# Kernel optimization log

Hardware: AMD Instinct MI355X
Metric: run time of the kernel (lower is better)

## Reference

```python
import jax, jax.numpy as jnp
import numpy as np

B, S, DM, H, SD = 8, 2048, 512, 8, 64
INNER = H * SD
HID = 4 * DM
EPS = 1e-5


def setup_inputs() -> dict:
    key = jax.random.key(0)
    ks = jax.random.split(key, 12)
    p = lambda k, sh: jax.random.normal(k, sh, dtype=jnp.float32) * 0.02
    return {
        "x": jax.random.normal(ks[0], (B, S, DM), dtype=jnp.float32),
        "norm_g": jnp.ones((DM,), jnp.float32),
        "norm_b": jnp.zeros((DM,), jnp.float32),
        "ffn_norm_g": jnp.ones((DM,), jnp.float32),
        "ffn_norm_b": jnp.zeros((DM,), jnp.float32),
        "Wa": p(ks[1], (INNER, DM)),
        "Wb": p(ks[2], (INNER, DM)),
        "Wql": p(ks[3], (INNER, DM)),
        "Wqr": p(ks[4], (INNER, DM)),
        "Wsd": p(ks[5], (H, DM)),
        "bsd": jnp.zeros((H,), jnp.float32),
        "Wpd": p(ks[6], (H, DM)),
        "bpd": jnp.zeros((H,), jnp.float32),
        "Wout": p(ks[7], (DM, INNER)),
        "W1": p(ks[8], (HID, DM)),
        "b1": jnp.zeros((HID,), jnp.float32),
        "W2": p(ks[9], (DM, HID)),
        "b2": jnp.zeros((DM,), jnp.float32),
    }


def _ln(x, g, b):
    m = x.mean(-1, keepdims=True)
    v = ((x - m) ** 2).mean(-1, keepdims=True)
    return (x - m) / jnp.sqrt(v + EPS) * g + b


def reference(x, norm_g, norm_b, ffn_norm_g, ffn_norm_b, Wa, Wb, Wql, Wqr,
              Wsd, bsd, Wpd, bpd, Wout, W1, b1, W2, b2):
    n = _ln(x, norm_g, norm_b)  # [B,S,DM]
    # project, reshape to heads, move time axis first for scan: [S,B,H,SD]
    tm = lambda t: t.reshape(B, S, H, SD).transpose(1, 0, 2, 3)
    a_all = tm(jnp.tanh(n @ Wa.T))
    b_all = tm(jnp.tanh(n @ Wb.T))
    ql_all = tm(jnp.tanh(n @ Wql.T))
    qr_all = tm(jnp.tanh(n @ Wqr.T))
    sd_all = jax.nn.sigmoid(n @ Wsd.T + bsd).transpose(1, 0, 2)[..., None]        # [S,B,H,1]
    pd_all = jax.nn.sigmoid(n @ Wpd.T + bpd).transpose(1, 0, 2)[..., None, None]  # [S,B,H,1,1]

    def step(carry, inp):
        state, pair = carry  # state [B,H,SD], pair [B,H,SD,SD]
        at, bt, qlt, sdt, pdt = inp
        prev = state
        state = sdt * state + (1.0 - sdt) * at
        pair = pdt * pair + (1.0 - pdt) * jnp.einsum('bhd,bhe->bhde', prev, bt)
        lc = jnp.einsum('bhde,bhd->bhe', pair, qlt)  # left context [B,H,SD]
        return (state, pair), lc

    init = (jnp.zeros((B, H, SD), x.dtype), jnp.zeros((B, H, SD, SD), x.dtype))
    _, lc = jax.lax.scan(step, init, (a_all, b_all, ql_all, sd_all, pd_all))  # [S,B,H,SD]

    mixed = ((lc * qr_all).transpose(1, 0, 2, 3).reshape(B, S, INNER)) @ Wout.T  # [B,S,DM]
    r = x + mixed  # dropout is identity in eval
    h = jax.nn.gelu(_ln(r, ffn_norm_g, ffn_norm_b) @ W1.T + b1, approximate=False)
    return r + h @ W2.T + b2
```

## Files before the change

### kernel.cpp

```cpp
#include <hip/hip_runtime.h>
#include <cstdint>
#include <cstddef>

#define B_    8
#define S_    2048
#define DM_   512
#define H_    8
#define SD_   64
#define HID_  2048
#define ROWS  (B_*S_)
#define BH    (B_*H_)
#define NCHUNK 32
#define CLEN   64
#define EPS_  1e-5f
#define PLANE ((size_t)ROWS*64)

typedef __bf16 bf16x8 __attribute__((ext_vector_type(8)));
typedef float  floatx4 __attribute__((ext_vector_type(4)));


static __device__ __forceinline__ float bf2f(unsigned short h){
  union { unsigned int u; float f; } v; v.u = ((unsigned int)h) << 16; return v.f;
}
static __device__ __forceinline__ unsigned short f2bf(float f){
  union { float f; unsigned int u; } v; v.f = f;
  unsigned int r = v.u + 0x7fffu + ((v.u >> 16) & 1u);
  return (unsigned short)(r >> 16);
}
static __device__ __forceinline__ float fast_tanh(float x){
  float ax = fabsf(x);
  float e  = __expf(2.f*ax);
  float t  = 1.f - 2.f/(e+1.f);
  return copysignf(t, x);
}
static __device__ __forceinline__ float sigmoidf_(float z){
  return 1.f/(1.f + expf(-z));
}
static __device__ __forceinline__ float gelu_exact(float x){
  return 0.5f*x*(1.f + erff(x*0.70710678118654752440f));
}
static __device__ __forceinline__ void gld_lds16(const unsigned short* g, unsigned short* lds){
  __builtin_amdgcn_global_load_lds(
      (const __attribute__((address_space(1))) void*)g,
      (__attribute__((address_space(3))) void*)lds,
      16, 0, 0);
}
static __device__ __forceinline__ int swz(int row, int col){
  return row*64 + (((col>>3) ^ (row&7))<<3) + (col&7);
}

__global__ __launch_bounds__(256) void cvt_weights(
    const float* __restrict__ wa, const float* __restrict__ wb,
    const float* __restrict__ wql, const float* __restrict__ wqr,
    const float* __restrict__ wout, const float* __restrict__ w1,
    const float* __restrict__ w2,
    unsigned short* __restrict__ wcat, unsigned short* __restrict__ woutb,
    unsigned short* __restrict__ w1b, unsigned short* __restrict__ w2b){
  int i = blockIdx.x*256 + threadIdx.x;
  const float* s; unsigned short* d; int base;
  if      (i <  65536){ s=wa;   d=wcat;          base=i; }
  else if (i < 131072){ s=wb;   d=wcat+262144;   base=i-65536; }
  else if (i < 196608){ s=wql;  d=wcat+524288;   base=i-131072; }
  else if (i < 262144){ s=wqr;  d=wcat+786432;   base=i-196608; }
  else if (i < 327680){ s=wout; d=woutb;         base=i-262144; }
  else if (i < 589824){ s=w1;   d=w1b;           base=i-327680; }
  else                { s=w2;   d=w2b;           base=i-589824; }
  float4 v = ((const float4*)s)[base];
  ushort4 o; o.x=f2bf(v.x); o.y=f2bf(v.y); o.z=f2bf(v.z); o.w=f2bf(v.w);
  ((ushort4*)d)[base] = o;
}

__global__ __launch_bounds__(256) void ln_gates(
    const float* __restrict__ x, const float* __restrict__ gam, const float* __restrict__ bet,
    const float* __restrict__ Wsd, const float* __restrict__ bsd,
    const float* __restrict__ Wpd, const float* __restrict__ bpd,
    unsigned short* __restrict__ nbf, float* __restrict__ sdo, float* __restrict__ pdo){
  const int row = blockIdx.x*4 + (threadIdx.x>>6), l = threadIdx.x & 63;
  const float* xr = x + (size_t)row*DM_;
  float4 v0 = ((const float4*)xr)[l*2];
  float4 v1 = ((const float4*)xr)[l*2+1];
  float v[8] = {v0.x,v0.y,v0.z,v0.w,v1.x,v1.y,v1.z,v1.w};
  float s = 0.f;
  #pragma unroll
  for (int i=0;i<8;++i) s += v[i];
  #pragma unroll
  for (int m=1;m<64;m<<=1) s += __shfl_xor(s, m);
  const float mean = s * (1.f/512.f);
  float q = 0.f;
  #pragma unroll
  for (int i=0;i<8;++i){ float d = v[i]-mean; q += d*d; }
  #pragma unroll
  for (int m=1;m<64;m<<=1) q += __shfl_xor(q, m);
  const float rstd = rsqrtf(q*(1.f/512.f) + EPS_);
  float4 g0 = ((const float4*)gam)[l*2], g1 = ((const float4*)gam)[l*2+1];
  float4 b0 = ((const float4*)bet)[l*2], b1 = ((const float4*)bet)[l*2+1];
  float gg[8] = {g0.x,g0.y,g0.z,g0.w,g1.x,g1.y,g1.z,g1.w};
  float bb[8] = {b0.x,b0.y,b0.z,b0.w,b1.x,b1.y,b1.z,b1.w};
  float n[8];
  #pragma unroll
  for (int i=0;i<8;++i) n[i] = (v[i]-mean)*rstd*gg[i] + bb[i];
  ushort4 o0, o1;
  o0.x=f2bf(n[0]); o0.y=f2bf(n[1]); o0.z=f2bf(n[2]); o0.w=f2bf(n[3]);
  o1.x=f2bf(n[4]); o1.y=f2bf(n[5]); o1.z=f2bf(n[6]); o1.w=f2bf(n[7]);
  ((ushort4*)(nbf + (size_t)row*DM_))[l*2]   = o0;
  ((ushort4*)(nbf + (size_t)row*DM_))[l*2+1] = o1;
  float acc[16];
  #pragma unroll
  for (int hh=0; hh<8; ++hh){
    const float4* ws = (const float4*)(Wsd + hh*DM_) + l*2;
    const float4* wp = (const float4*)(Wpd + hh*DM_) + l*2;
    float4 a0=ws[0], a1=ws[1], p0=wp[0], p1=wp[1];
    acc[hh]   = n[0]*a0.x+n[1]*a0.y+n[2]*a0.z+n[3]*a0.w+n[4]*a1.x+n[5]*a1.y+n[6]*a1.z+n[7]*a1.w;
    acc[8+hh] = n[0]*p0.x+n[1]*p0.y+n[2]*p0.z+n[3]*p0.w+n[4]*p1.x+n[5]*p1.y+n[6]*p1.z+n[7]*p1.w;
  }
  #pragma unroll
  for (int k=0;k<16;++k){
    float a = acc[k];
    #pragma unroll
    for (int m=1;m<64;m<<=1) a += __shfl_xor(a, m);
    acc[k] = a;
  }
  if (l==0){
    #pragma unroll
    for (int hh=0; hh<8; ++hh){
      sdo[(size_t)hh*ROWS + row] = sigmoidf_(acc[hh]   + bsd[hh]);
      pdo[(size_t)hh*ROWS + row] = sigmoidf_(acc[8+hh] + bpd[hh]);
    }
  }
}

__global__ __launch_bounds__(256) void ln_plain(
    const unsigned short* __restrict__ xb, const float* __restrict__ gam, const float* __restrict__ bet,
    unsigned short* __restrict__ ob){
  const int row = blockIdx.x*4 + (threadIdx.x>>6), l = threadIdx.x & 63;
  const unsigned short* xr = xb + (size_t)row*DM_ + l*8;
  ushort4 u0 = *(const ushort4*)xr;
  ushort4 u1 = *(const ushort4*)(xr+4);
  float v[8] = {bf2f(u0.x),bf2f(u0.y),bf2f(u0.z),bf2f(u0.w),
                bf2f(u1.x),bf2f(u1.y),bf2f(u1.z),bf2f(u1.w)};
  float s = 0.f;
  #pragma unroll
  for (int i=0;i<8;++i) s += v[i];
  #pragma unroll
  for (int m=1;m<64;m<<=1) s += __shfl_xor(s, m);
  const float mean = s * (1.f/512.f);
  float q = 0.f;
  #pragma unroll
  for (int i=0;i<8;++i){ float d = v[i]-mean; q += d*d; }
  #pragma unroll
  for (int m=1;m<64;m<<=1) q += __shfl_xor(q, m);
  const float rstd = rsqrtf(q*(1.f/512.f) + EPS_);
  float4 g0 = ((const float4*)gam)[l*2], g1 = ((const float4*)gam)[l*2+1];
  float4 b0 = ((const float4*)bet)[l*2], b1 = ((const float4*)bet)[l*2+1];
  float gg[8] = {g0.x,g0.y,g0.z,g0.w,g1.x,g1.y,g1.z,g1.w};
  float bb[8] = {b0.x,b0.y,b0.z,b0.w,b1.x,b1.y,b1.z,b1.w};
  ushort4 o0, o1;
  o0.x=f2bf((v[0]-mean)*rstd*gg[0]+bb[0]); o0.y=f2bf((v[1]-mean)*rstd*gg[1]+bb[1]);
  o0.z=f2bf((v[2]-mean)*rstd*gg[2]+bb[2]); o0.w=f2bf((v[3]-mean)*rstd*gg[3]+bb[3]);
  o1.x=f2bf((v[4]-mean)*rstd*gg[4]+bb[4]); o1.y=f2bf((v[5]-mean)*rstd*gg[5]+bb[5]);
  o1.z=f2bf((v[6]-mean)*rstd*gg[6]+bb[6]); o1.w=f2bf((v[7]-mean)*rstd*gg[7]+bb[7]);
  ((ushort4*)(ob + (size_t)row*DM_))[l*2]   = o0;
  ((ushort4*)(ob + (size_t)row*DM_))[l*2+1] = o1;
}

template<int MODE>
__global__ __launch_bounds__(256) void gemm128(
    const unsigned short* __restrict__ A, const unsigned short* __restrict__ W,
    const float* __restrict__ bias, const float* __restrict__ residf,
    const unsigned short* __restrict__ residb,
    float* __restrict__ outf, unsigned short* __restrict__ outb,
    int N, int K){
  __shared__ __align__(16) unsigned short As[128*64];
  __shared__ __align__(16) unsigned short Ws[128*64];
  const int tid  = threadIdx.x;
  const int w    = tid >> 6;
  const int lane = tid & 63;
  const int mblk = blockIdx.x, nblk = blockIdx.y;
  const int mrow = (w >> 1) * 64;
  const int ncol = (w & 1) * 64;
  const int fr = lane & 15, fq = lane >> 4;

  int srow[4], scol[4];
  #pragma unroll
  for (int q=0;q<4;++q){
    const int p = q*256 + w*64 + lane;
    srow[q] = p >> 3;
    scol[q] = ((p & 7) ^ (srow[q] & 7)) * 8;
  }

  floatx4 acc[4][4];
  #pragma unroll
  for (int i=0;i<4;++i)
    #pragma unroll
    for (int j=0;j<4;++j)
      acc[i][j] = (floatx4){0.f,0.f,0.f,0.f};

  for (int k0=0; k0<K; k0+=64){
    #pragma unroll
    for (int q=0;q<4;++q){
      gld_lds16(A + (size_t)(mblk*128 + srow[q])*K + k0 + scol[q], As + (q*256 + w*64)*8);
      gld_lds16(W + (size_t)(nblk*128 + srow[q])*K + k0 + scol[q], Ws + (q*256 + w*64)*8);
    }
    __syncthreads();
    #pragma unroll
    for (int kh=0;kh<2;++kh){
      bf16x8 af[4], bf[4];
      #pragma unroll
      for (int i=0;i<4;++i) af[i] = *(const bf16x8*)&As[swz(mrow + i*16 + fr, kh*32 + fq*8)];
      #pragma unroll
      for (int j=0;j<4;++j) bf[j] = *(const bf16x8*)&Ws[swz(ncol + j*16 + fr, kh*32 + fq*8)];
      #pragma unroll
      for (int i=0;i<4;++i)
        #pragma unroll
        for (int j=0;j<4;++j)
          acc[i][j] = __builtin_amdgcn_mfma_f32_16x16x32_bf16(af[i], bf[j], acc[i][j], 0, 0, 0);
    }
    __syncthreads();
  }

  #pragma unroll
  for (int i=0;i<4;++i){
    const int grow_base = mblk*128 + mrow + i*16 + fq*4;
    #pragma unroll
    for (int j=0;j<4;++j){
      const int gcol = nblk*128 + ncol + j*16 + fr;
      float bias_v = 0.f;
      if (MODE==2 || MODE==3) bias_v = bias[gcol];
      #pragma unroll
      for (int r=0;r<4;++r){
        float v = acc[i][j][r];
        if (MODE==0){
          const size_t o = (size_t)(gcol>>6)*PLANE + (size_t)(grow_base + r)*64 + (gcol & 63);
          outb[o] = f2bf(fast_tanh(v));
        } else {
          const size_t o = (size_t)(grow_base + r)*N + gcol;
          if      (MODE==1) outb[o] = f2bf(residf[o] + v);
          else if (MODE==2) outb[o] = f2bf(gelu_exact(v + bias_v));
          else              outf[o] = bf2f(residb[o]) + v + bias_v;
        }
      }
    }
  }
}

__global__ __launch_bounds__(64) void state_local(
    const unsigned short* __restrict__ proj, const float* __restrict__ sdo,
    unsigned short* __restrict__ slocb, float* __restrict__ Sarr,
    float* __restrict__ sEnd){
  __shared__ __align__(16) unsigned short a_s[4096];
  __shared__ float sv_s[64];
  const int c = blockIdx.x, bh = blockIdx.y, b = bh>>3, h = bh&7, d = threadIdx.x;
  const int t0 = c*CLEN;
  const unsigned short* ap = proj + (size_t)h*PLANE + (size_t)(b*S_+t0)*64;
  #pragma unroll
  for (int q=0;q<8;++q)
    *(float4*)&a_s[(q*64 + d)*8] = *(const float4*)(ap + (size_t)(q*64 + d)*8);
  sv_s[d] = sdo[(size_t)h*ROWS + b*S_+t0+d];
  __syncthreads();
  float s = 0.f, S = 1.f;
  #pragma unroll 4
  for (int j=0;j<CLEN;++j){
    const int t = t0 + j;
    float a  = bf2f(a_s[j*64 + d]);
    float sv = sv_s[j];
    s = sv*s + (1.f-sv)*a;
    S *= sv;
    slocb[((size_t)bh*S_ + t)*64 + d] = f2bf(s);
    if (d==0) Sarr[bh*S_ + t] = S;
  }
  sEnd[((size_t)c*BH + bh)*64 + d] = s;
}

__global__ __launch_bounds__(64) void state_combine(
    const float* __restrict__ sEnd, const float* __restrict__ Sarr,
    float* __restrict__ sinit){
  const int bh = blockIdx.x, d = threadIdx.x;
  float acc = 0.f;
  for (int c=0;c<NCHUNK;++c){
    sinit[((size_t)c*BH + bh)*64 + d] = acc;
    const int te = c*CLEN + CLEN - 1;
    acc = Sarr[bh*S_ + te]*acc + sEnd[((size_t)c*BH + bh)*64 + d];
  }
}

__global__ __launch_bounds__(128) void pair_localm(
    const unsigned short* __restrict__ proj, const float* __restrict__ pdo,
    const unsigned short* __restrict__ slocb, const float* __restrict__ Sarr,
    const float* __restrict__ sinit, float* __restrict__ pairbuf,
    float* __restrict__ Dprod){
  __shared__ __align__(16) unsigned short Bt[4096];
  __shared__ __align__(16) unsigned short Pt[4096];
  const int c=blockIdx.x, bh=blockIdx.y, b=bh>>3, h=bh&7;
  const int w = threadIdx.x>>6, l = threadIdx.x&63;
  const int t = c*CLEN + l;
  float pd = pdo[(size_t)h*ROWS + b*S_+t];
  float D = pd;
  #pragma unroll
  for (int m=1;m<64;m<<=1){ float o = __shfl_up(D, m); if (l>=m) D *= o; }
  const float Dend = __shfl(D, 63);
  const float cu = (Dend / D) * (1.f - pd);
  if (w==0 && l==63) Dprod[c*BH+bh] = Dend;
  {
    const unsigned short* brow = proj + (size_t)(8+h)*PLANE + (size_t)(b*S_+t)*64;
    const size_t ptm = (size_t)bh*S_ + (l==0 ? t : t-1);
    const unsigned short* srow = slocb + ptm*64;
    const float* initp = sinit + ((size_t)c*BH + bh)*64;
    float sp = 0.f;
    if (l>0) sp = Sarr[ptm];
    #pragma unroll
    for (int e8=w*4; e8<w*4+4; ++e8){
      ushort4 u0 = *(const ushort4*)(brow + e8*8);
      ushort4 u1 = *(const ushort4*)(brow + e8*8 + 4);
      unsigned short vs[8] = {u0.x,u0.y,u0.z,u0.w,u1.x,u1.y,u1.z,u1.w};
      ushort4 s0 = *(const ushort4*)(srow + e8*8);
      ushort4 s1 = *(const ushort4*)(srow + e8*8 + 4);
      unsigned short ss[8] = {s0.x,s0.y,s0.z,s0.w,s1.x,s1.y,s1.z,s1.w};
      float4 i0 = *(const float4*)(initp + e8*8);
      float4 i1 = *(const float4*)(initp + e8*8 + 4);
      float iv[8] = {i0.x,i0.y,i0.z,i0.w,i1.x,i1.y,i1.z,i1.w};
      #pragma unroll
      for (int q=0;q<8;++q){
        const int r = e8*8+q;
        float p = (l==0) ? iv[q] : (sp*iv[q] + bf2f(ss[q]));
        Bt[swz(r, l)] = f2bf(cu * bf2f(vs[q]));
        Pt[swz(r, l)] = f2bf(p);
      }
    }
  }
  __syncthreads();
  const int fr = l & 15, fq = l >> 4;
  floatx4 acc[4][2];
  #pragma unroll
  for (int i=0;i<4;++i)
    #pragma unroll
    for (int jj=0;jj<2;++jj) acc[i][jj] = (floatx4){0.f,0.f,0.f,0.f};
  #pragma unroll
  for (int kh=0;kh<2;++kh){
    bf16x8 af[4], bfr[2];
    #pragma unroll
    for (int i=0;i<4;++i)  af[i]  = *(const bf16x8*)&Bt[swz(i*16+fr, kh*32+fq*8)];
    #pragma unroll
    for (int jj=0;jj<2;++jj) bfr[jj] = *(const bf16x8*)&Pt[swz((w*2+jj)*16+fr, kh*32+fq*8)];
    #pragma unroll
    for (int i=0;i<4;++i)
      #pragma unroll
      for (int jj=0;jj<2;++jj)
        acc[i][jj] = __builtin_amdgcn_mfma_f32_16x16x32_bf16(af[i], bfr[jj], acc[i][jj], 0, 0, 0);
  }
  float* outp = pairbuf + ((size_t)c*BH + bh)*4096;
  #pragma unroll
  for (int i=0;i<4;++i)
    #pragma unroll
    for (int jj=0;jj<2;++jj)
      #pragma unroll
      for (int r=0;r<4;++r)
        outp[(i*16+fq*4+r)*64 + (w*2+jj)*16+fr] = acc[i][jj][r];
}

__global__ __launch_bounds__(256) void pair_combine(
    const float* __restrict__ pairbuf, const float* __restrict__ Dprod,
    unsigned short* __restrict__ pinitb){
  const int idx = blockIdx.x*256 + threadIdx.x;
  const int de = idx & 4095, bh = idx >> 12;
  float acc = 0.f;
  for (int c=0;c<NCHUNK;++c){
    const size_t o = ((size_t)c*BH + bh)*4096 + de;
    pinitb[o] = f2bf(acc);
    acc = Dprod[c*BH + bh]*acc + pairbuf[o];
  }
}

__global__ __launch_bounds__(128) void pair_finalm(
    const unsigned short* __restrict__ proj, const float* __restrict__ pdo,
    const unsigned short* __restrict__ slocb, const float* __restrict__ Sarr,
    const float* __restrict__ sinit, const unsigned short* __restrict__ pinitb,
    unsigned short* __restrict__ lcqr){
  __shared__ __align__(16) unsigned short Bt[4096];
  __shared__ __align__(16) unsigned short Tb[4096];
  __shared__ __align__(16) float Dtl[64];
  __shared__ __align__(16) float cudl[64];
  const int c=blockIdx.x, bh=blockIdx.y, b=bh>>3, h=bh&7;
  const int w=threadIdx.x>>6, l=threadIdx.x&63;
  const int t0 = c*CLEN;
  const int trow = t0 + l;
  float pd = pdo[(size_t)h*ROWS + b*S_+trow];
  float D = pd;
  #pragma unroll
  for (int m=1;m<64;m<<=1){ float o = __shfl_up(D, m); if (l>=m) D *= o; }
  if (w==0){ Dtl[l] = D; cudl[l] = (1.f - pd) / D; }
  {
    const unsigned short* brow = proj + (size_t)(8+h)*PLANE + (size_t)(b*S_+trow)*64;
    #pragma unroll
    for (int e8=w*4; e8<w*4+4; ++e8){
      ushort4 u0 = *(const ushort4*)(brow + e8*8);
      ushort4 u1 = *(const ushort4*)(brow + e8*8 + 4);
      unsigned short vs[8] = {u0.x,u0.y,u0.z,u0.w,u1.x,u1.y,u1.z,u1.w};
      #pragma unroll
      for (int q=0;q<8;++q) Bt[swz(e8*8+q, l)] = vs[q];
    }
  }
  __syncthreads();
  const int fr = l & 15, fq = l >> 4;
  const float* initp = sinit + ((size_t)c*BH + bh)*64;
  bf16x8 qf[4][2], pf[2][2];
  #pragma unroll
  for (int i=0;i<4;++i)
    #pragma unroll
    for (int kh=0;kh<2;++kh)
      qf[i][kh] = *(const bf16x8*)(proj + (size_t)(16+h)*PLANE + (size_t)(b*S_ + t0 + i*16 + fr)*64 + kh*32 + fq*8);
  #pragma unroll
  for (int jw=0;jw<2;++jw){
    const int jx = w*2+jw;
    const int tr = t0 + jx*16 + fr;
    const bool first = (jx==0 && fr==0);
    const size_t ptm = (size_t)bh*S_ + (first ? tr : tr-1);
    float sp = 0.f;
    if (!first) sp = Sarr[ptm];
    #pragma unroll
    for (int kh=0;kh<2;++kh){
      bf16x8 sv = *(const bf16x8*)(slocb + ptm*64 + kh*32 + fq*8);
      float4 i0 = *(const float4*)(initp + kh*32 + fq*8);
      float4 i1 = *(const float4*)(initp + kh*32 + fq*8 + 4);
      float iv[8] = {i0.x,i0.y,i0.z,i0.w,i1.x,i1.y,i1.z,i1.w};
      bf16x8 pv;
      #pragma unroll
      for (int e=0;e<8;++e){
        float p = first ? iv[e] : (sp*iv[e] + (float)sv[e]);
        pv[e] = (__bf16)p;
      }
      pf[jw][kh] = pv;
    }
  }
  floatx4 sacc[4][2];
  #pragma unroll
  for (int i=0;i<4;++i)
    #pragma unroll
    for (int jw=0;jw<2;++jw) sacc[i][jw] = (floatx4){0.f,0.f,0.f,0.f};
  #pragma unroll
  for (int kh=0;kh<2;++kh)
    #pragma unroll
    for (int i=0;i<4;++i)
      #pragma unroll
      for (int jw=0;jw<2;++jw)
        sacc[i][jw] = __builtin_amdgcn_mfma_f32_16x16x32_bf16(qf[i][kh], pf[jw][kh], sacc[i][jw], 0, 0, 0);
  float mycud[2];
  #pragma unroll
  for (int jw=0;jw<2;++jw) mycud[jw] = cudl[(w*2+jw)*16+fr];
  #pragma unroll
  for (int i=0;i<4;++i){
    floatx4 dtv = *(const floatx4*)&Dtl[i*16+fq*4];
    #pragma unroll
    for (int jw=0;jw<2;++jw){
      const int uu = (w*2+jw)*16+fr;
      #pragma unroll
      for (int r=0;r<4;++r){
        const int tt = i*16+fq*4+r;
        float v = (uu<=tt) ? (sacc[i][jw][r]*dtv[r])*mycud[jw] : 0.f;
        Tb[swz(tt, uu)] = f2bf(v);
      }
    }
  }
  __syncthreads();
  floatx4 acc[4][2];
  #pragma unroll
  for (int i=0;i<4;++i)
    #pragma unroll
    for (int jw=0;jw<2;++jw) acc[i][jw] = (floatx4){0.f,0.f,0.f,0.f};
  #pragma unroll
  for (int kh=0;kh<2;++kh){
    bf16x8 af[4], bfr[2];
    #pragma unroll
    for (int i=0;i<4;++i)  af[i]  = *(const bf16x8*)&Tb[swz(i*16+fr, kh*32+fq*8)];
    #pragma unroll
    for (int jw=0;jw<2;++jw) bfr[jw] = *(const bf16x8*)&Bt[swz((w*2+jw)*16+fr, kh*32+fq*8)];
    #pragma unroll
    for (int i=0;i<4;++i)
      #pragma unroll
      for (int jw=0;jw<2;++jw)
        acc[i][jw] = __builtin_amdgcn_mfma_f32_16x16x32_bf16(af[i], bfr[jw], acc[i][jw], 0, 0, 0);
  }
  {
    const unsigned short* ib = pinitb + ((size_t)c*BH + bh)*4096;
    #pragma unroll
    for (int kh=0;kh<2;++kh){
      bf16x8 qs[4], inf[2];
      #pragma unroll
      for (int i=0;i<4;++i){
        const float sc = Dtl[i*16+fr];
        #pragma unroll
        for (int e=0;e<8;++e) qs[i][e] = (__bf16)(sc * (float)qf[i][kh][e]);
      }
      #pragma unroll
      for (int jw=0;jw<2;++jw)
        inf[jw] = *(const bf16x8*)(ib + ((w*2+jw)*16+fr)*64 + kh*32 + fq*8);
      #pragma unroll
      for (int i=0;i<4;++i)
        #pragma unroll
        for (int jw=0;jw<2;++jw)
          acc[i][jw] = __builtin_amdgcn_mfma_f32_16x16x32_bf16(qs[i], inf[jw], acc[i][jw], 0, 0, 0);
    }
  }
  __syncthreads();
  #pragma unroll
  for (int i=0;i<4;++i)
    #pragma unroll
    for (int jw=0;jw<2;++jw)
      #pragma unroll
      for (int r=0;r<4;++r)
        Tb[swz(i*16+fq*4+r, (w*2+jw)*16+fr)] = f2bf(acc[i][jw][r]);
  __syncthreads();
  {
    const unsigned short* qrow = proj + (size_t)(24+h)*PLANE + (size_t)(b*S_+trow)*64;
    unsigned short* orow = lcqr + ((size_t)(b*S_+trow))*512 + h*64;
    #pragma unroll
    for (int e8=w*4; e8<w*4+4; ++e8){
      bf16x8 lcv = *(const bf16x8*)&Tb[swz(l, e8*8)];
      ushort4 q0 = *(const ushort4*)(qrow + e8*8);
      ushort4 q1 = *(const ushort4*)(qrow + e8*8 + 4);
      unsigned short qv[8] = {q0.x,q0.y,q0.z,q0.w,q1.x,q1.y,q1.z,q1.w};
      ushort4 o0, o1;
      o0.x = f2bf((float)lcv[0]*bf2f(qv[0]));
      o0.y = f2bf((float)lcv[1]*bf2f(qv[1]));
      o0.z = f2bf((float)lcv[2]*bf2f(qv[2]));
      o0.w = f2bf((float)lcv[3]*bf2f(qv[3]));
      o1.x = f2bf((float)lcv[4]*bf2f(qv[4]));
      o1.y = f2bf((float)lcv[5]*bf2f(qv[5]));
      o1.z = f2bf((float)lcv[6]*bf2f(qv[6]));
      o1.w = f2bf((float)lcv[7]*bf2f(qv[7]));
      *(ushort4*)(orow + e8*8)     = o0;
      *(ushort4*)(orow + e8*8 + 4) = o1;
    }
  }
}

extern "C" void kernel_launch(void* const* d_in, const int* in_sizes, int n_in,
                              void* d_out, int out_size, void* d_ws, size_t ws_size,
                              hipStream_t stream){
  (void)in_sizes; (void)n_in; (void)out_size; (void)ws_size;
  const float* x    = (const float*)d_in[0];
  const float* ng   = (const float*)d_in[1];
  const float* nb   = (const float*)d_in[2];
  const float* fng  = (const float*)d_in[3];
  const float* fnb  = (const float*)d_in[4];
  const float* Wa   = (const float*)d_in[5];
  const float* Wb   = (const float*)d_in[6];
  const float* Wql  = (const float*)d_in[7];
  const float* Wqr  = (const float*)d_in[8];
  const float* Wsd  = (const float*)d_in[9];
  const float* bsd  = (const float*)d_in[10];
  const float* Wpd  = (const float*)d_in[11];
  const float* bpd  = (const float*)d_in[12];
  const float* Wout = (const float*)d_in[13];
  const float* W1   = (const float*)d_in[14];
  const float* b1   = (const float*)d_in[15];
  const float* W2   = (const float*)d_in[16];
  const float* b2   = (const float*)d_in[17];
  float* out = (float*)d_out;
  char* ws = (char*)d_ws;

  size_t off = 0;
  auto alloc = [&](size_t bytes)->char*{ char* p = ws + off; off += (bytes + 255) & ~(size_t)255; return p; };
  char* RA = alloc((size_t)ROWS*DM_*2);
  char* RB = alloc((size_t)ROWS*2048*2);
  char* RD = alloc((size_t)NCHUNK*BH*4096*4);
  char* RE = alloc((size_t)BH*S_*64*4);
  float* sdo   = (float*)alloc((size_t)ROWS*8*4);
  float* pdo   = (float*)alloc((size_t)ROWS*8*4);
  float* Sarr  = (float*)alloc((size_t)BH*S_*4);
  float* sinit = (float*)alloc((size_t)NCHUNK*BH*64*4);
  float* sEnd  = (float*)alloc((size_t)NCHUNK*BH*64*4);
  float* dprod = (float*)alloc((size_t)NCHUNK*BH*4);
  unsigned short* wcat  = (unsigned short*)alloc((size_t)2048*512*2);
  unsigned short* woutb = (unsigned short*)alloc((size_t)512*512*2);
  unsigned short* w1b   = (unsigned short*)alloc((size_t)2048*512*2);
  unsigned short* w2b   = (unsigned short*)alloc((size_t)512*2048*2);

  unsigned short* nbf   = (unsigned short*)RA;
  unsigned short* lcqr  = (unsigned short*)RA;
  unsigned short* nr    = (unsigned short*)RA;
  unsigned short* proj  = (unsigned short*)RB;
  unsigned short* hbuf  = (unsigned short*)RB;
  float* pairb = (float*)RD;
  unsigned short* slocb  = (unsigned short*)RE;
  unsigned short* rbufb  = (unsigned short*)RE;
  unsigned short* pinitb = (unsigned short*)(RE + (size_t)BH*S_*64*2);

  cvt_weights<<<dim3(3328), dim3(256), 0, stream>>>(Wa,Wb,Wql,Wqr,Wout,W1,W2, wcat,woutb,w1b,w2b);
  ln_gates<<<dim3(ROWS/4), dim3(256), 0, stream>>>(x, ng, nb, Wsd, bsd, Wpd, bpd, nbf, sdo, pdo);
  gemm128<0><<<dim3(128,16), dim3(256), 0, stream>>>(nbf, wcat, nullptr, nullptr, nullptr, nullptr, proj, 2048, 512);
  state_local<<<dim3(NCHUNK,BH), dim3(64), 0, stream>>>(proj, sdo, slocb, Sarr, sEnd);
  state_combine<<<dim3(BH), dim3(64), 0, stream>>>(sEnd, Sarr, sinit);
  pair_localm<<<dim3(NCHUNK,BH), dim3(128), 0, stream>>>(proj, pdo, slocb, Sarr, sinit, pairb, dprod);
  pair_combine<<<dim3(1024), dim3(256), 0, stream>>>(pairb, dprod, pinitb);
  pair_finalm<<<dim3(NCHUNK,BH), dim3(128), 0, stream>>>(proj, pdo, slocb, Sarr, sinit, pinitb, lcqr);
  gemm128<1><<<dim3(128,4), dim3(256), 0, stream>>>(lcqr, woutb, nullptr, x, nullptr, nullptr, rbufb, 512, 512);
  ln_plain<<<dim3(ROWS/4), dim3(256), 0, stream>>>(rbufb, fng, fnb, nr);
  gemm128<2><<<dim3(128,16), dim3(256), 0, stream>>>(nr, w1b, b1, nullptr, nullptr, nullptr, hbuf, 2048, 512);
  gemm128<3><<<dim3(128,4), dim3(256), 0, stream>>>(hbuf, w2b, b2, nullptr, rbufb, out, nullptr, 512, 2048);
}
```

Measured before the change: 404.0 us.

## Add dedicated triple-buffered 256x128 GEMM for FFN down-projection

```diff
diff --git a/kernel.cpp b/kernel.cpp
--- a/kernel.cpp
+++ b/kernel.cpp
@@ -238,6 +238,160 @@
           else if (MODE==2) outb[o] = f2bf(gelu_exact(v + bias_v));
           else              outf[o] = bf2f(residb[o]) + v + bias_v;
         }
+      }
+    }
+  }
+}
+
+__global__ __launch_bounds__(512, 2) void gemm_ffn2(
+    const unsigned short* __restrict__ A, const unsigned short* __restrict__ W,
+    const float* __restrict__ bias, const unsigned short* __restrict__ residb,
+    float* __restrict__ outf, int N, int K){
+  __shared__ __align__(16) unsigned short lds[73728];
+  const int tid  = threadIdx.x;
+  const int w    = tid >> 6;
+  const int lane = tid & 63;
+  const int mrow = (w >> 2) * 128;
+  const int ncol = (w & 3) * 32;
+  const int fr = lane & 15, fq = lane >> 4;
+  const int mblk = blockIdx.x, nblk = blockIdx.y;
+  const int nt = K >> 6;
+
+  int srA[4], scA[4];
+  #pragma unroll
+  for (int q=0;q<4;++q){
+    const int p = q*512 + tid;
+    srA[q] = p >> 3;
+    scA[q] = ((p & 7) ^ (srA[q] & 7)) * 8;
+  }
+  int srW[2], scW[2];
+  #pragma unroll
+  for (int q=0;q<2;++q){
+    const int p = q*512 + tid;
+    srW[q] = p >> 3;
+    scW[q] = ((p & 7) ^ (srW[q] & 7)) * 8;
+  }
+  const unsigned short* Ag = A + (size_t)(mblk*256)*K;
+  const unsigned short* Wg = W + (size_t)(nblk*128)*K;
+
+  floatx4 acc[8][2];
+  #pragma unroll
+  for (int i=0;i<8;++i)
+    #pragma unroll
+    for (int j=0;j<2;++j) acc[i][j] = (floatx4){0.f,0.f,0.f,0.f};
+
+  #pragma unroll
+  for (int q=0;q<4;++q)
+    gld_lds16(Ag + (size_t)srA[q]*K + scA[q], lds + (q*512 + w*64)*8);
+  #pragma unroll
+  for (int q=0;q<2;++q)
+    gld_lds16(Wg + (size_t)srW[q]*K + scW[q], lds + 16384 + (q*512 + w*64)*8);
+  #pragma unroll
+  for (int q=0;q<4;++q)
+    gld_lds16(Ag + (size_t)srA[q]*K + 64 + scA[q], lds + 24576 + (q*512 + w*64)*8);
+  #pragma unroll
+  for (int q=0;q<2;++q)
+    gld_lds16(Wg + (size_t)srW[q]*K + 64 + scW[q], lds + 24576 + 16384 + (q*512 + w*64)*8);
+
+  int buf = 0;
+  for (int t=0; t<nt; ++t){
+    unsigned short* As  = lds + buf*24576;
+    unsigned short* Wst = As + 16384;
+    int nb2 = buf + 2; if (nb2 >= 3) nb2 -= 3;
+    unsigned short* Sb  = lds + nb2*24576;
+    const bool st = (t + 2 < nt);
+    const int k2 = (t + 2) << 6;
+
+    if (t == nt-1) asm volatile("s_waitcnt vmcnt(0)" ::: "memory");
+    else           asm volatile("s_waitcnt vmcnt(6)" ::: "memory");
+    __builtin_amdgcn_s_barrier();
+
+    bf16x8 af[4][2], bf[2][2];
+    #pragma unroll
+    for (int i=0;i<4;++i){
+      const int row = mrow + i*16 + fr;
+      af[i][0] = *(const bf16x8*)&As[swz(row, fq*8)];
+      af[i][1] = *(const bf16x8*)&As[swz(row, 32 + fq*8)];
+    }
+    #pragma unroll
+    for (int j=0;j<2;++j){
+      const int row = ncol + j*16 + fr;
+      bf[j][0] = *(const bf16x8*)&Wst[swz(row, fq*8)];
+      bf[j][1] = *(const bf16x8*)&Wst[swz(row, 32 + fq*8)];
+    }
+    if (st){
+      gld_lds16(Ag + (size_t)srA[0]*K + k2 + scA[0], Sb + (0*512 + w*64)*8);
+      gld_lds16(Ag + (size_t)srA[1]*K + k2 + scA[1], Sb + (1*512 + w*64)*8);
+    }
+    __builtin_amdgcn_s_barrier();
+    asm volatile("s_waitcnt lgkmcnt(0)" ::: "memory");
+    __builtin_amdgcn_sched_barrier(0);
+    __builtin_amdgcn_s_setprio(1);
+    #pragma unroll
+    for (int i=0;i<4;++i)
+      #pragma unroll
+      for (int j=0;j<2;++j)
+        acc[i][j] = __builtin_amdgcn_mfma_f32_16x16x32_bf16(af[i][0], bf[j][0], acc[i][j], 0, 0, 0);
+    __builtin_amdgcn_s_setprio(0);
+    __builtin_amdgcn_s_barrier();
+
+    if (st){
+      gld_lds16(Ag + (size_t)srA[2]*K + k2 + scA[2], Sb + (2*512 + w*64)*8);
+      gld_lds16(Ag + (size_t)srA[3]*K + k2 + scA[3], Sb + (3*512 + w*64)*8);
+    }
+    __builtin_amdgcn_s_setprio(1);
+    #pragma unroll
+    for (int i=0;i<4;++i)
+      #pragma unroll
+      for (int j=0;j<2;++j)
+        acc[i][j] = __builtin_amdgcn_mfma_f32_16x16x32_bf16(af[i][1], bf[j][1], acc[i][j], 0, 0, 0);
+    __builtin_amdgcn_s_setprio(0);
+    __builtin_amdgcn_s_barrier();
+
+    #pragma unroll
+    for (int i=0;i<4;++i){
+      const int row = mrow + 64 + i*16 + fr;
+      af[i][0] = *(const bf16x8*)&As[swz(row, fq*8)];
+      af[i][1] = *(const bf16x8*)&As[swz(row, 32 + fq*8)];
+    }
+    if (st){
+      gld_lds16(Wg + (size_t)srW[0]*K + k2 + scW[0], Sb + 16384 + (0*512 + w*64)*8);
+      gld_lds16(Wg + (size_t)srW[1]*K + k2 + scW[1], Sb + 16384 + (1*512 + w*64)*8);
+    }
+    __builtin_amdgcn_s_barrier();
+    asm volatile("s_waitcnt lgkmcnt(0)" ::: "memory");
+    __builtin_amdgcn_sched_barrier(0);
+    __builtin_amdgcn_s_setprio(1);
+    #pragma unroll
+    for (int i=0;i<4;++i)
+      #pragma unroll
+      for (int j=0;j<2;++j)
+        acc[4+i][j] = __builtin_amdgcn_mfma_f32_16x16x32_bf16(af[i][0], bf[j][0], acc[4+i][j], 0, 0, 0);
+    __builtin_amdgcn_s_setprio(0);
+    __builtin_amdgcn_s_barrier();
+
+    __builtin_amdgcn_s_setprio(1);
+    #pragma unroll
+    for (int i=0;i<4;++i)
+      #pragma unroll
+      for (int j=0;j<2;++j)
+        acc[4+i][j] = __builtin_amdgcn_mfma_f32_16x16x32_bf16(af[i][1], bf[j][1], acc[4+i][j], 0, 0, 0);
+    __builtin_amdgcn_s_setprio(0);
+
+    buf = (buf == 2) ? 0 : buf + 1;
+  }
+
+  #pragma unroll
+  for (int i=0;i<8;++i){
+    const int grow_base = mblk*256 + mrow + (i>>2)*64 + (i&3)*16 + fq*4;
+    #pragma unroll
+    for (int j=0;j<2;++j){
+      const int gcol = nblk*128 + ncol + j*16 + fr;
+      const float bias_v = bias[gcol];
+      #pragma unroll
+      for (int r=0;r<4;++r){
+        const size_t o = (size_t)(grow_base + r)*N + gcol;
+        outf[o] = bf2f(residb[o]) + acc[i][j][r] + bias_v;
       }
     }
   }
@@ -596,5 +750,5 @@
   gemm128<1><<<dim3(128,4), dim3(256), 0, stream>>>(lcqr, woutb, nullptr, x, nullptr, nullptr, rbufb, 512, 512);
   ln_plain<<<dim3(ROWS/4), dim3(256), 0, stream>>>(rbufb, fng, fnb, nr);
   gemm128<2><<<dim3(128,16), dim3(256), 0, stream>>>(nr, w1b, b1, nullptr, nullptr, nullptr, hbuf, 2048, 512);
-  gemm128<3><<<dim3(128,4), dim3(256), 0, stream>>>(hbuf, w2b, b2, nullptr, rbufb, out, nullptr, 512, 2048);
-}
+  gemm_ffn2<<<dim3(64,4), dim3(512), 0, stream>>>(hbuf, w2b, b2, rbufb, out, 512, 2048);
+}
```

New measurement: 403.7 us. About the same (-0.1%).
